# Kernel optimization log

Hardware: AMD Instinct MI355X
Metric: run time of the kernel (lower is better)

## Reference

```python
import jax, jax.numpy as jnp
import numpy as np

D_COEF = 1e-05   # diffusivity (init arg D)
DX = 1e-04       # mesh spacing (init arg mesh.dx)
NX = 4_194_304   # grid points


def setup_inputs() -> dict:
    key = jax.random.key(0)
    C = jax.random.uniform(key, (NX,), dtype=jnp.float32)
    dt = jnp.asarray(0.1, dtype=jnp.float32)
    C_surf = jnp.asarray(1.0, dtype=jnp.float32)
    C_bulk = jnp.asarray(0.0, dtype=jnp.float32)
    return {"C": C, "dt": dt, "C_surf": C_surf, "C_bulk": C_bulk}


def reference(C, dt, C_surf, C_bulk):
    """Backward-Euler implicit step: solve (I - dt*D*Lap) C_next = C via Thomas algorithm."""
    nx = C.shape[0]
    dtype = C.dtype
    dt = jnp.asarray(dt, dtype=dtype)
    dx = jnp.asarray(DX, dtype=dtype)
    Dc = jnp.asarray(D_COEF, dtype=dtype)
    C_surf = jnp.asarray(C_surf, dtype=dtype)
    C_bulk = jnp.asarray(C_bulk, dtype=dtype)
    one = jnp.asarray(1.0, dtype=dtype)
    two = jnp.asarray(2.0, dtype=dtype)
    zero = jnp.asarray(0.0, dtype=dtype)

    r = Dc * dt / dx ** 2
    # Tridiagonal system: sub-diag a (len nx-1), diag b (len nx), super-diag c (len nx-1), rhs d
    a = jnp.full((nx - 1,), -r, dtype=dtype)
    b = jnp.full((nx,), one + two * r, dtype=dtype)
    c = jnp.full((nx - 1,), -r, dtype=dtype)
    d = jnp.copy(C)
    # Dirichlet BC at x=0
    b = b.at[0].set(one)
    c = c.at[0].set(zero)
    d = d.at[0].set(C_surf)
    # Dirichlet BC at x=L
    a = a.at[-1].set(zero)
    b = b.at[-1].set(one)
    d = d.at[-1].set(C_bulk)

    # Forward sweep (sequential recurrence)
    def forward_sweep(carry, elems):
        c_prime_prev, d_prime_prev = carry
        a_i, b_i, c_i, d_i = elems
        denom = b_i - a_i * c_prime_prev
        c_prime = c_i / denom
        d_prime = (d_i - a_i * d_prime_prev) / denom
        return (c_prime, d_prime), (c_prime, d_prime)

    a_padded = jnp.concatenate([jnp.array([zero], dtype=dtype), a])
    c_padded = jnp.concatenate([c, jnp.array([zero], dtype=dtype)])
    denom_0 = b[0]
    c_prime_0 = c_padded[0] / denom_0
    d_prime_0 = d[0] / denom_0
    _, (c_prime_arr, d_prime_arr) = jax.lax.scan(
        forward_sweep, (c_prime_0, d_prime_0),
        (a_padded[1:], b[1:], c_padded[1:], d[1:]))
    c_prime_arr = jnp.concatenate([jnp.array([c_prime_0], dtype=dtype), c_prime_arr])
    d_prime_arr = jnp.concatenate([jnp.array([d_prime_0], dtype=dtype), d_prime_arr])

    # Backward substitution (sequential recurrence)
    def backward_sweep(x_next, elems):
        c_prime_i, d_prime_i = elems
        x_i = d_prime_i - c_prime_i * x_next
        return x_i, x_i

    _, x_rev = jax.lax.scan(
        backward_sweep, d_prime_arr[-1],
        (c_prime_arr[:-1][::-1], d_prime_arr[:-1][::-1]))
    x = jnp.concatenate([x_rev[::-1], jnp.array([d_prime_arr[-1]], dtype=dtype)])
    return x
```

## Files before the change

kernel.cpp:

```cpp
#include <hip/hip_runtime.h>
#include <math.h>

#define NTH   256
#define T_PER 10
#define HALO  256
#define NDATA (NTH * T_PER)
#define CHUNK (NDATA - 2 * HALO)

__global__ void __launch_bounds__(NTH, 4)
diffusion_thomas(const float* __restrict__ C, const float* __restrict__ dtp,
                 const float* __restrict__ csp, const float* __restrict__ cbp,
                 float* __restrict__ out, int n)
{
    __shared__ __align__(16) float s[NDATA];
    __shared__ float waggF[4], waggB[4], sPL, sPR;

    const int tid  = threadIdx.x;
    const int lane = tid & 63;
    const int w    = tid >> 6;
    const int bs   = (int)blockIdx.x * CHUNK;
    const int wbase = bs - HALO;
    const bool isB0   = (blockIdx.x == 0);
    const bool isLast = (blockIdx.x == gridDim.x - 1);

    const float dt = dtp[0], Cs = csp[0], Cb = cbp[0];
    const double rd    = 1e-5 * (double)dt / (1e-4 * 1e-4);
    const double sq    = sqrt(1.0 + 4.0 * rd);
    const double betad = 2.0 * rd / ((1.0 + 2.0 * rd) + sq);
    const double g0d   = 1.0 / ((1.0 + 2.0 * rd) - 2.0 * rd * betad);
    const double b2 = betad*betad, b4 = b2*b2, b8 = b4*b4, b10 = b8*b2;
    const double a2 = b10*b10, a4 = a2*a2, a8 = a4*a4, a16 = a8*a8, a32 = a16*a16;
    const double b640 = a32*a32;
    const float beta = (float)betad, G0 = (float)g0d, r = (float)rd;
    const float lbeta = (float)log(betad);
    const float A1=(float)b10, A2=(float)a2, A4=(float)a4,
                A8=(float)a8, A16=(float)a16, A32=(float)a32, B640=(float)b640;

    for (int k4 = tid; k4 < NDATA / 4; k4 += NTH) {
        int g0 = wbase + 4 * k4;
        float4 v;
        if (g0 >= 2 && g0 + 3 <= n - 3) {
            v = *reinterpret_cast<const float4*>(C + g0);
        } else {
            float t0[4];
#pragma unroll
            for (int e = 0; e < 4; ++e) {
                int g = g0 + e; float x = 0.0f;
                if (g >= 1 && g <= n - 2) {
                    x = C[g];
                    if (g == 1)     x = fmaf(r, Cs, x);
                    if (g == n - 2) x = fmaf(r, Cb, x);
                }
                t0[e] = x;
            }
            v = make_float4(t0[0], t0[1], t0[2], t0[3]);
        }
        *reinterpret_cast<float4*>(&s[4 * k4]) = v;
    }
    __syncthreads();

    const int l0 = tid * T_PER;
    float d[T_PER];
#pragma unroll
    for (int j = 0; j < T_PER; ++j) d[j] = s[l0 + j];
    float Sf = 0.0f, Sb = 0.0f;
#pragma unroll
    for (int j = 0; j < T_PER; ++j) {
        Sf = fmaf(beta, Sf, d[j]);
        Sb = fmaf(beta, Sb, d[T_PER - 1 - j]);
    }

    float c = Sf, cbk = Sb, u;
    u = __shfl_up(c, 1);    if (lane >= 1)  c = fmaf(A1,  u, c);
    u = __shfl_up(c, 2);    if (lane >= 2)  c = fmaf(A2,  u, c);
    u = __shfl_up(c, 4);    if (lane >= 4)  c = fmaf(A4,  u, c);
    u = __shfl_up(c, 8);    if (lane >= 8)  c = fmaf(A8,  u, c);
    u = __shfl_up(c, 16);   if (lane >= 16) c = fmaf(A16, u, c);
    u = __shfl_up(c, 32);   if (lane >= 32) c = fmaf(A32, u, c);
    u = __shfl_down(cbk, 1);  if (lane <= 62) cbk = fmaf(A1,  u, cbk);
    u = __shfl_down(cbk, 2);  if (lane <= 61) cbk = fmaf(A2,  u, cbk);
    u = __shfl_down(cbk, 4);  if (lane <= 59) cbk = fmaf(A4,  u, cbk);
    u = __shfl_down(cbk, 8);  if (lane <= 55) cbk = fmaf(A8,  u, cbk);
    u = __shfl_down(cbk, 16); if (lane <= 47) cbk = fmaf(A16, u, cbk);
    u = __shfl_down(cbk, 32); if (lane <= 31) cbk = fmaf(A32, u, cbk);

    if (lane == 63) waggF[w] = c;
    if (lane == 0)  waggB[w] = cbk;
    __syncthreads();

    float Cw = 0.0f;
    for (int wp = 0; wp < w; ++wp)  Cw  = fmaf(B640, Cw,  waggF[wp]);
    float CwB = 0.0f;
    for (int wp = 3; wp > w; --wp)  CwB = fmaf(B640, CwB, waggB[wp]);

    float cup = __shfl_up(c, 1);
    float carryF = (lane == 0) ? Cw
                 : fmaf(__expf(lbeta * (float)(T_PER * lane)), Cw, cup);
    float cdn = __shfl_down(cbk, 1);
    float carryB = (lane == 63) ? CwB
                 : fmaf(__expf(lbeta * (float)(T_PER * (63 - lane))), CwB, cdn);

    float F[T_PER];
    float f = carryF;
#pragma unroll
    for (int j = 0; j < T_PER; ++j) {
        f = fmaf(beta, f, d[j]);
        F[j] = f;
        if (isLast && (wbase + l0 + j) == n - 2) sPR = G0 * beta * f;
    }

    float b = carryB;
#pragma unroll
    for (int j = T_PER - 1; j >= 0; --j) {
        b = fmaf(beta, b, d[j]);
        if (isB0 && (l0 + j) == HALO) sPL = G0 * b;
        F[j] = G0 * (F[j] + b - d[j]);
    }

    __syncthreads();

    if (isB0) {
        float PL = sPL;
#pragma unroll
        for (int j = 0; j < T_PER; ++j) {
            int i = l0 + j - HALO;
            if (i >= 1 && i < 512)
                F[j] = fmaf(-__expf(lbeta * (float)i), PL, F[j]);
            if (i == 0) F[j] = Cs;
        }
    }
    if (isLast) {
        float PR = sPR;
#pragma unroll
        for (int j = 0; j < T_PER; ++j) {
            int g = wbase + l0 + j;
            if (g >= n - 512 && g <= n - 2)
                F[j] = fmaf(-__expf(lbeta * (float)(n - 1 - g)), PR, F[j]);
            if (g == n - 1) F[j] = Cb;
        }
    }

#pragma unroll
    for (int j = 0; j < T_PER; ++j) s[l0 + j] = F[j];
    __syncthreads();
    for (int k4 = tid; k4 < CHUNK / 4; k4 += NTH) {
        int g0 = bs + 4 * k4;
        float4 v = *reinterpret_cast<const float4*>(&s[HALO + 4 * k4]);
        if (g0 + 3 < n) {
            *reinterpret_cast<float4*>(out + g0) = v;
        } else {
            if (g0     < n) out[g0]     = v.x;
            if (g0 + 1 < n) out[g0 + 1] = v.y;
            if (g0 + 2 < n) out[g0 + 2] = v.z;
            if (g0 + 3 < n) out[g0 + 3] = v.w;
        }
    }
}

extern "C" void kernel_launch(void* const* d_in, const int* in_sizes, int n_in,
                              void* d_out, int out_size, void* d_ws, size_t ws_size,
                              hipStream_t stream) {
    const float* C  = (const float*)d_in[0];
    const float* dt = (const float*)d_in[1];
    const float* cs = (const float*)d_in[2];
    const float* cb = (const float*)d_in[3];
    float* out = (float*)d_out;
    const int n  = in_sizes[0];
    const int nb = (n + CHUNK - 1) / CHUNK;
    diffusion_thomas<<<nb, NTH, 0, stream>>>(C, dt, cs, cb, out, n);
}
```

Before: 78.38 us.

## Drop shared-memory staging, widen per-thread segments and shrink halo

Each thread now loads its 16-element segment directly from global memory into registers with float4 loads and writes results straight back, so the shared-memory staging, its copy loops and most barriers are gone. The per-thread segment grows from 10 to 16 elements and the halo drops from 256 to 128, which cuts the redundant overlap work per block. The cross-wave carry now uses only the neighbouring wave's aggregate, relying on the decay of beta raised to large powers. In exchange, truncation error from the shorter halo and carry is larger, and the per-thread strided global accesses are less coalesced.

```diff
diff --git a/kernel.cpp b/kernel.cpp
--- a/kernel.cpp
+++ b/kernel.cpp
@@ -2,24 +2,26 @@
 #include <math.h>
 
 #define NTH   256
-#define T_PER 10
-#define HALO  256
+#define T_PER 16
+#define HALO  128
 #define NDATA (NTH * T_PER)
 #define CHUNK (NDATA - 2 * HALO)
+#define NWAVE (NTH / 64)
 
 __global__ void __launch_bounds__(NTH, 4)
-diffusion_thomas(const float* __restrict__ C, const float* __restrict__ dtp,
-                 const float* __restrict__ csp, const float* __restrict__ cbp,
-                 float* __restrict__ out, int n)
+diffusion_scan(const float* __restrict__ C, const float* __restrict__ dtp,
+               const float* __restrict__ csp, const float* __restrict__ cbp,
+               float* __restrict__ out, int n)
 {
-    __shared__ __align__(16) float s[NDATA];
-    __shared__ float waggF[4], waggB[4], sPL, sPR;
+    __shared__ float waggF[NWAVE], waggB[NWAVE];
+    __shared__ float sPL, sPR;
 
-    const int tid  = threadIdx.x;
-    const int lane = tid & 63;
-    const int w    = tid >> 6;
-    const int bs   = (int)blockIdx.x * CHUNK;
+    const int tid   = threadIdx.x;
+    const int lane  = tid & 63;
+    const int w     = tid >> 6;
+    const int bs    = (int)blockIdx.x * CHUNK;
     const int wbase = bs - HALO;
+    const int seg0  = wbase + tid * T_PER;
     const bool isB0   = (blockIdx.x == 0);
     const bool isLast = (blockIdx.x == gridDim.x - 1);
 
@@ -28,41 +30,38 @@
     const double sq    = sqrt(1.0 + 4.0 * rd);
     const double betad = 2.0 * rd / ((1.0 + 2.0 * rd) + sq);
     const double g0d   = 1.0 / ((1.0 + 2.0 * rd) - 2.0 * rd * betad);
-    const double b2 = betad*betad, b4 = b2*b2, b8 = b4*b4, b10 = b8*b2;
-    const double a2 = b10*b10, a4 = a2*a2, a8 = a4*a4, a16 = a8*a8, a32 = a16*a16;
-    const double b640 = a32*a32;
+    const double b2 = betad * betad, b4 = b2 * b2, b8 = b4 * b4;
+    const double s16 = b8 * b8;
+    const double s32 = s16 * s16, s64 = s32 * s32, s128 = s64 * s64;
     const float beta = (float)betad, G0 = (float)g0d, r = (float)rd;
     const float lbeta = (float)log(betad);
-    const float A1=(float)b10, A2=(float)a2, A4=(float)a4,
-                A8=(float)a8, A16=(float)a16, A32=(float)a32, B640=(float)b640;
+    const float A1 = (float)s16, A2 = (float)s32, A4 = (float)s64, A8 = (float)s128;
 
-    for (int k4 = tid; k4 < NDATA / 4; k4 += NTH) {
-        int g0 = wbase + 4 * k4;
-        float4 v;
-        if (g0 >= 2 && g0 + 3 <= n - 3) {
-            v = *reinterpret_cast<const float4*>(C + g0);
-        } else {
-            float t0[4];
+    float d[T_PER];
+    const bool interior = (seg0 >= 2) && (seg0 + T_PER <= n - 2);
+    if (interior) {
 #pragma unroll
-            for (int e = 0; e < 4; ++e) {
-                int g = g0 + e; float x = 0.0f;
-                if (g >= 1 && g <= n - 2) {
-                    x = C[g];
-                    if (g == 1)     x = fmaf(r, Cs, x);
-                    if (g == n - 2) x = fmaf(r, Cb, x);
-                }
-                t0[e] = x;
+        for (int q = 0; q < T_PER / 4; ++q) {
+            float4 v = *reinterpret_cast<const float4*>(C + seg0 + 4 * q);
+            d[4 * q]     = v.x;
+            d[4 * q + 1] = v.y;
+            d[4 * q + 2] = v.z;
+            d[4 * q + 3] = v.w;
+        }
+    } else {
+#pragma unroll
+        for (int j = 0; j < T_PER; ++j) {
+            int g = seg0 + j;
+            float x = 0.0f;
+            if (g >= 1 && g <= n - 2) {
+                x = C[g];
+                if (g == 1)     x = fmaf(r, Cs, x);
+                if (g == n - 2) x = fmaf(r, Cb, x);
             }
-            v = make_float4(t0[0], t0[1], t0[2], t0[3]);
+            d[j] = x;
         }
-        *reinterpret_cast<float4*>(&s[4 * k4]) = v;
     }
-    __syncthreads();
 
-    const int l0 = tid * T_PER;
-    float d[T_PER];
-#pragma unroll
-    for (int j = 0; j < T_PER; ++j) d[j] = s[l0 + j];
     float Sf = 0.0f, Sb = 0.0f;
 #pragma unroll
     for (int j = 0; j < T_PER; ++j) {
@@ -71,34 +70,27 @@
     }
 
     float c = Sf, cbk = Sb, u;
-    u = __shfl_up(c, 1);    if (lane >= 1)  c = fmaf(A1,  u, c);
-    u = __shfl_up(c, 2);    if (lane >= 2)  c = fmaf(A2,  u, c);
-    u = __shfl_up(c, 4);    if (lane >= 4)  c = fmaf(A4,  u, c);
-    u = __shfl_up(c, 8);    if (lane >= 8)  c = fmaf(A8,  u, c);
-    u = __shfl_up(c, 16);   if (lane >= 16) c = fmaf(A16, u, c);
-    u = __shfl_up(c, 32);   if (lane >= 32) c = fmaf(A32, u, c);
-    u = __shfl_down(cbk, 1);  if (lane <= 62) cbk = fmaf(A1,  u, cbk);
-    u = __shfl_down(cbk, 2);  if (lane <= 61) cbk = fmaf(A2,  u, cbk);
-    u = __shfl_down(cbk, 4);  if (lane <= 59) cbk = fmaf(A4,  u, cbk);
-    u = __shfl_down(cbk, 8);  if (lane <= 55) cbk = fmaf(A8,  u, cbk);
-    u = __shfl_down(cbk, 16); if (lane <= 47) cbk = fmaf(A16, u, cbk);
-    u = __shfl_down(cbk, 32); if (lane <= 31) cbk = fmaf(A32, u, cbk);
+    u = __shfl_up(c, 1);   if (lane >= 1) c = fmaf(A1, u, c);
+    u = __shfl_up(c, 2);   if (lane >= 2) c = fmaf(A2, u, c);
+    u = __shfl_up(c, 4);   if (lane >= 4) c = fmaf(A4, u, c);
+    u = __shfl_up(c, 8);   if (lane >= 8) c = fmaf(A8, u, c);
+    u = __shfl_down(cbk, 1);  if (lane <= 62) cbk = fmaf(A1, u, cbk);
+    u = __shfl_down(cbk, 2);  if (lane <= 61) cbk = fmaf(A2, u, cbk);
+    u = __shfl_down(cbk, 4);  if (lane <= 59) cbk = fmaf(A4, u, cbk);
+    u = __shfl_down(cbk, 8);  if (lane <= 55) cbk = fmaf(A8, u, cbk);
 
     if (lane == 63) waggF[w] = c;
     if (lane == 0)  waggB[w] = cbk;
     __syncthreads();
+    const float Cw  = (w > 0)         ? waggF[w - 1] : 0.0f;
+    const float CwB = (w < NWAVE - 1) ? waggB[w + 1] : 0.0f;
 
-    float Cw = 0.0f;
-    for (int wp = 0; wp < w; ++wp)  Cw  = fmaf(B640, Cw,  waggF[wp]);
-    float CwB = 0.0f;
-    for (int wp = 3; wp > w; --wp)  CwB = fmaf(B640, CwB, waggB[wp]);
-
-    float cup = __shfl_up(c, 1);
-    float carryF = (lane == 0) ? Cw
-                 : fmaf(__expf(lbeta * (float)(T_PER * lane)), Cw, cup);
-    float cdn = __shfl_down(cbk, 1);
-    float carryB = (lane == 63) ? CwB
-                 : fmaf(__expf(lbeta * (float)(T_PER * (63 - lane))), CwB, cdn);
+    const float cup = __shfl_up(c, 1);
+    const float carryF = (lane == 0)
+        ? Cw : fmaf(__expf(lbeta * (float)(T_PER * lane)), Cw, cup);
+    const float cdn = __shfl_down(cbk, 1);
+    const float carryB = (lane == 63)
+        ? CwB : fmaf(__expf(lbeta * (float)(T_PER * (63 - lane))), CwB, cdn);
 
     float F[T_PER];
     float f = carryF;
@@ -106,53 +98,57 @@
     for (int j = 0; j < T_PER; ++j) {
         f = fmaf(beta, f, d[j]);
         F[j] = f;
-        if (isLast && (wbase + l0 + j) == n - 2) sPR = G0 * beta * f;
+    }
+    if (isLast) {
+#pragma unroll
+        for (int j = 0; j < T_PER; ++j)
+            if (seg0 + j == n - 2) sPR = G0 * beta * F[j];
     }
 
     float b = carryB;
 #pragma unroll
     for (int j = T_PER - 1; j >= 0; --j) {
         b = fmaf(beta, b, d[j]);
-        if (isB0 && (l0 + j) == HALO) sPL = G0 * b;
+        if (isB0 && (seg0 + j) == 0) sPL = G0 * b;
         F[j] = G0 * (F[j] + b - d[j]);
     }
 
-    __syncthreads();
-
-    if (isB0) {
-        float PL = sPL;
+    if (isB0 || isLast) {
+        __syncthreads();
+        if (isB0) {
+            const float PL = sPL;
 #pragma unroll
-        for (int j = 0; j < T_PER; ++j) {
-            int i = l0 + j - HALO;
-            if (i >= 1 && i < 512)
-                F[j] = fmaf(-__expf(lbeta * (float)i), PL, F[j]);
-            if (i == 0) F[j] = Cs;
+            for (int j = 0; j < T_PER; ++j) {
+                int i = seg0 + j;
+                if (i >= 1 && i < 512)
+                    F[j] = fmaf(-__expf(lbeta * (float)i), PL, F[j]);
+                if (i == 0) F[j] = Cs;
+            }
         }
-    }
-    if (isLast) {
-        float PR = sPR;
+        if (isLast) {
+            const float PR = sPR;
 #pragma unroll
-        for (int j = 0; j < T_PER; ++j) {
-            int g = wbase + l0 + j;
-            if (g >= n - 512 && g <= n - 2)
-                F[j] = fmaf(-__expf(lbeta * (float)(n - 1 - g)), PR, F[j]);
-            if (g == n - 1) F[j] = Cb;
+            for (int j = 0; j < T_PER; ++j) {
+                int g = seg0 + j;
+                if (g >= n - 512 && g <= n - 2)
+                    F[j] = fmaf(-__expf(lbeta * (float)(n - 1 - g)), PR, F[j]);
+                if (g == n - 1) F[j] = Cb;
+            }
         }
     }
 
+    if (tid >= HALO / T_PER && tid < (HALO + CHUNK) / T_PER && seg0 < n) {
+        if (seg0 + T_PER <= n) {
 #pragma unroll
-    for (int j = 0; j < T_PER; ++j) s[l0 + j] = F[j];
-    __syncthreads();
-    for (int k4 = tid; k4 < CHUNK / 4; k4 += NTH) {
-        int g0 = bs + 4 * k4;
-        float4 v = *reinterpret_cast<const float4*>(&s[HALO + 4 * k4]);
-        if (g0 + 3 < n) {
-            *reinterpret_cast<float4*>(out + g0) = v;
+            for (int q = 0; q < T_PER / 4; ++q) {
+                float4 v = make_float4(F[4 * q], F[4 * q + 1],
+                                       F[4 * q + 2], F[4 * q + 3]);
+                *reinterpret_cast<float4*>(out + seg0 + 4 * q) = v;
+            }
         } else {
-            if (g0     < n) out[g0]     = v.x;
-            if (g0 + 1 < n) out[g0 + 1] = v.y;
-            if (g0 + 2 < n) out[g0 + 2] = v.z;
-            if (g0 + 3 < n) out[g0 + 3] = v.w;
+#pragma unroll
+            for (int j = 0; j < T_PER; ++j)
+                if (seg0 + j < n) out[seg0 + j] = F[j];
         }
     }
 }
@@ -167,5 +163,5 @@
     float* out = (float*)d_out;
     const int n  = in_sizes[0];
     const int nb = (n + CHUNK - 1) / CHUNK;
-    diffusion_thomas<<<nb, NTH, 0, stream>>>(C, dt, cs, cb, out, n);
+    diffusion_scan<<<nb, NTH, 0, stream>>>(C, dt, cs, cb, out, n);
 }
```

Result: slower. 81.05 us (+3.4%).
